# Kernel tuning notes

Measured on AMD Instinct MI355X. Metric: run time of the kernel, lower is better.

Reference implementation:

```python
import jax, jax.numpy as jnp
import numpy as np

EPS = 1e-6  # torch.nn.PairwiseDistance default eps: dist = ||x - y + eps||_2


def setup_inputs() -> dict:
    key = jax.random.key(0)
    k1, k2 = jax.random.split(key)
    samples = jax.random.normal(k1, (4096, 128), dtype=jnp.float32)   # batch of observations
    V = jax.random.uniform(k2, (65536, 128), dtype=jnp.float32)       # grown node codebook (torch.rand init)
    return {"samples": samples, "V": V}


def reference(samples, V):
    # activate_bmu, vectorized over the batch.
    # torch PairwiseDistance(p=2): d_n = || x - V_n + eps ||_2
    D = samples.shape[-1]
    x_sq = jnp.sum(samples * samples, axis=-1)        # [B]
    v_sq = jnp.sum(V * V, axis=-1)                    # [N]
    xv = jnp.einsum('bd,nd->bn', samples, V)          # [B, N]
    x_sum = jnp.sum(samples, axis=-1)                 # [B]
    v_sum = jnp.sum(V, axis=-1)                       # [N]
    sq = (x_sq[:, None] + v_sq[None, :] - 2.0 * xv
          + 2.0 * EPS * (x_sum[:, None] - v_sum[None, :]) + D * EPS * EPS)
    dists = jnp.sqrt(jnp.maximum(sq, 0.0))            # [B, N]
    # top-2 smallest distances -> BMU b, second BMU s
    neg_top2, idx = jax.lax.top_k(-dists, 2)          # [B, 2]
    b = idx[:, 0]
    s = idx[:, 1]
    a = jnp.exp(neg_top2[:, 0])                       # exp(-b_dist)
    return (b, s, a)
```

## Files before the change

### kernel.cpp

```cpp
#include <hip/hip_runtime.h>
#include <math.h>

#define NS 4096
#define NV 65536
#define DDIM 128
#define EPSV 1e-6f
#define NCHUNK 16
#define TILES_PER_CHUNK 32
#define NTILE 512
#define FLTMAX 3.402823466e+38f
#define IMAX 0x7fffffff

#define XSQ_F    0
#define XSUM_F   4096
#define PART_F   8192
#define D12_F    270336
#define T12_I    278528
#define CELL1_I  286720
#define CELL2_I  290816
#define WS_TILED_BYTE 1605632
#define TILE_BYTES 65536
#define TILE_STRIDE 66560

typedef __attribute__((ext_vector_type(8)))  __bf16        bf16x8;
typedef __attribute__((ext_vector_type(8)))  unsigned short ush8;
typedef __attribute__((ext_vector_type(4)))  unsigned short ush4;
typedef __attribute__((ext_vector_type(16))) float          f32x16;

typedef const __attribute__((address_space(1))) unsigned int* gp_t;
typedef __attribute__((address_space(3))) unsigned int*       lp_t;

__device__ __forceinline__ void async_cp16(const void* g, void* l) {
    __builtin_amdgcn_global_load_lds((gp_t)g, (lp_t)l, 16, 0, 0);
}

__device__ __forceinline__ unsigned short f2bf(float x) {
    unsigned u = __builtin_bit_cast(unsigned, x);
    u += 0x7FFFu + ((u >> 16) & 1u);
    return (unsigned short)(u >> 16);
}
__device__ __forceinline__ float bf2f(unsigned short h) {
    unsigned u = ((unsigned)h) << 16;
    return __builtin_bit_cast(float, u);
}

__device__ __forceinline__ void merge2t(float& d1, int& i1, float& d2, int& i2,
                                        float d, int i) {
    bool b1 = (d < d1) || (d == d1 && i < i1);
    bool b2 = (d < d2) || (d == d2 && i < i2);
    if (b1) { d2 = d1; i2 = i1; d1 = d; i1 = i; }
    else if (b2) { d2 = d; i2 = i; }
}

__device__ __forceinline__ void load_bfrag(const float* __restrict__ samples,
                                           int srow, int q, ush8* bh, ush8* bl) {
    const float4* s4 = (const float4*)samples;
    #pragma unroll
    for (int s = 0; s < 8; s++) {
        float4 x0 = s4[(size_t)srow * 32 + s * 4 + q * 2];
        float4 x1 = s4[(size_t)srow * 32 + s * 4 + q * 2 + 1];
        float xs[8] = {x0.x, x0.y, x0.z, x0.w, x1.x, x1.y, x1.z, x1.w};
        #pragma unroll
        for (int j = 0; j < 8; j++) {
            float y = -2.0f * xs[j];
            unsigned short hh = f2bf(y);
            bh[s][j] = hh;
            bl[s][j] = f2bf(y - bf2f(hh));
        }
    }
}

__device__ __forceinline__ void tile_mfma(const char* __restrict__ lds,
                                          const ush8* bh, const ush8* bl,
                                          int q, int l31, f32x16 acc[4]) {
    #pragma unroll
    for (int mi = 0; mi < 4; mi++) {
        const char* cjb = lds + TILE_BYTES + (size_t)(mi * 32 + 4 * q) * 4;
        float4 c0 = *(const float4*)(cjb);
        float4 c1 = *(const float4*)(cjb + 32);
        float4 c2 = *(const float4*)(cjb + 64);
        float4 c3 = *(const float4*)(cjb + 96);
        acc[mi][0] = c0.x;  acc[mi][1] = c0.y;  acc[mi][2] = c0.z;  acc[mi][3] = c0.w;
        acc[mi][4] = c1.x;  acc[mi][5] = c1.y;  acc[mi][6] = c1.z;  acc[mi][7] = c1.w;
        acc[mi][8] = c2.x;  acc[mi][9] = c2.y;  acc[mi][10] = c2.z; acc[mi][11] = c2.w;
        acc[mi][12] = c3.x; acc[mi][13] = c3.y; acc[mi][14] = c3.z; acc[mi][15] = c3.w;
    }
    #pragma unroll
    for (int s = 0; s < 8; s++) {
        bf16x8 bhs = __builtin_bit_cast(bf16x8, bh[s]);
        bf16x8 bls = __builtin_bit_cast(bf16x8, bl[s]);
        #pragma unroll
        for (int mi = 0; mi < 4; mi++) {
            bf16x8 ah = *(const bf16x8*)(lds + (size_t)((((s * 2 + 0) * 2 + q) * 128) + mi * 32 + l31) * 16);
            bf16x8 al = *(const bf16x8*)(lds + (size_t)((((s * 2 + 1) * 2 + q) * 128) + mi * 32 + l31) * 16);
            acc[mi] = __builtin_amdgcn_mfma_f32_32x32x16_bf16(ah, bhs, acc[mi], 0, 0, 0);
            acc[mi] = __builtin_amdgcn_mfma_f32_32x32x16_bf16(ah, bls, acc[mi], 0, 0, 0);
            acc[mi] = __builtin_amdgcn_mfma_f32_32x32x16_bf16(al, bhs, acc[mi], 0, 0, 0);
        }
    }
}

__global__ void vq_prep(const float* __restrict__ samples,
                        const float* __restrict__ V,
                        char* __restrict__ ws) {
    __shared__ float tf[128 * 132];
    float* ws_f = (float*)ws;
    const int b = blockIdx.x;
    const int tid = threadIdx.x;
    if (b >= NV / 128) {
        int row = (b - NV / 128) * 4 + (tid >> 6);
        int lane = tid & 63;
        float2 v = ((const float2*)(samples + (size_t)row * DDIM))[lane];
        float s = v.x + v.y;
        float q = v.x * v.x + v.y * v.y;
        #pragma unroll
        for (int off = 32; off >= 1; off >>= 1) {
            s += __shfl_xor(s, off);
            q += __shfl_xor(q, off);
        }
        if (lane == 0) { ws_f[XSQ_F + row] = q; ws_f[XSUM_F + row] = s; }
        return;
    }
    const int tile = b;
    char* dst = ws + WS_TILED_BYTE + (size_t)tile * TILE_STRIDE;
    const float4* v4 = (const float4*)V;
    #pragma unroll
    for (int i = 0; i < 16; i++) {
        int flat = i * 256 + tid;
        int row = flat >> 5;
        int c4 = flat & 31;
        float4 g = v4[(size_t)(tile * 128 + row) * 32 + c4];
        *(float4*)&tf[row * 132 + c4 * 4] = g;
        float s = g.x + g.y + g.z + g.w;
        float q2 = g.x * g.x + g.y * g.y + g.z * g.z + g.w * g.w;
        #pragma unroll
        for (int off = 16; off >= 1; off >>= 1) {
            s += __shfl_xor(s, off);
            q2 += __shfl_xor(q2, off);
        }
        if ((tid & 31) == 0)
            *(float*)(dst + TILE_BYTES + row * 4) = q2 - 2.0f * EPSV * s;
    }
    __syncthreads();
    #pragma unroll
    for (int i = 0; i < 8; i++) {
        int task = i * 256 + tid;
        int row = task & 127;
        int sq = task >> 7;
        int s = sq >> 1, q = sq & 1;
        float4 lo = *(const float4*)&tf[row * 132 + s * 16 + q * 8];
        float4 hi = *(const float4*)&tf[row * 132 + s * 16 + q * 8 + 4];
        float xs[8] = {lo.x, lo.y, lo.z, lo.w, hi.x, hi.y, hi.z, hi.w};
        ush8 h, l;
        #pragma unroll
        for (int j = 0; j < 8; j++) {
            unsigned short hh = f2bf(xs[j]);
            h[j] = hh;
            l[j] = f2bf(xs[j] - bf2f(hh));
        }
        *(ush8*)(dst + (size_t)((((s * 2 + 0) * 2 + q) * 128) + row) * 16) = h;
        *(ush8*)(dst + (size_t)((((s * 2 + 1) * 2 + q) * 128) + row) * 16) = l;
    }
}

__device__ __forceinline__ void stage_tile512(const char* src, char* l, int tid) {
    #pragma unroll
    for (int i = 0; i < 8; i++) {
        int off = (i * 512 + tid) * 16;
        async_cp16(src + off, l + off);
    }
    if (tid < 64) {
        int off = TILE_BYTES + tid * 16;
        async_cp16(src + off, l + off);
    }
}

__global__ __launch_bounds__(512, 2)
void vq_gemm_topk(const float* __restrict__ samples, char* __restrict__ ws) {
    __shared__ __align__(16) char lds[2][TILE_STRIDE];
    const int tid = threadIdx.x;
    const int w = tid >> 6, lane = tid & 63;
    const int l31 = lane & 31, qb = lane >> 5;
    const int bid = blockIdx.x;
    const int g = bid >> 3;
    const int chunk = (bid & 7) * 2 + (g >> 4);
    const int st = g & 15;
    const int nrow = st * 256 + w * 32 + l31;

    const char* vbase = ws + WS_TILED_BYTE;
    const int tbase = chunk * TILES_PER_CHUNK;

    stage_tile512(vbase + (size_t)tbase * TILE_STRIDE, lds[0], tid);
    ush8 bh[8], bl[8];
    load_bfrag(samples, nrow, qb, bh, bl);
    __syncthreads();

    float D1 = FLTMAX, D2 = FLTMAX;
    int T1 = IMAX, T2 = IMAX;

    #pragma unroll 1
    for (int it = 0; it < TILES_PER_CHUNK; it++) {
        const int cur = it & 1;
        if (it + 1 < TILES_PER_CHUNK)
            stage_tile512(vbase + (size_t)(tbase + it + 1) * TILE_STRIDE,
                          lds[cur ^ 1], tid);
        f32x16 acc[4];
        tile_mfma(lds[cur], bh, bl, qb, l31, acc);
        float t1[4], t2[4];
        #pragma unroll
        for (int mi = 0; mi < 4; mi++) {
            t1[mi] = FLTMAX; t2[mi] = FLTMAX;
            #pragma unroll
            for (int r = 0; r < 16; r++) {
                float v = acc[mi][r];
                t2[mi] = fminf(t2[mi], fmaxf(t1[mi], v));
                t1[mi] = fminf(t1[mi], v);
            }
        }
        float tt1 = t1[0], tt2 = t2[0];
        #pragma unroll
        for (int mi = 1; mi < 4; mi++) {
            float tmp = fmaxf(tt1, t1[mi]);
            tt1 = fminf(tt1, t1[mi]);
            tt2 = fminf(fminf(tmp, tt2), t2[mi]);
        }
        const int tile = tbase + it;
        bool c1 = tt1 < D1;
        float m1 = fminf(D1, tt2);
        float m2 = fminf(D2, tt1);
        int T2a = (tt2 < D1) ? tile : T1;
        int T2b = (tt1 < D2) ? tile : T2;
        D2 = c1 ? m1 : m2;
        T2 = c1 ? T2a : T2b;
        T1 = c1 ? tile : T1;
        D1 = c1 ? tt1 : D1;
        __syncthreads();
    }

    {
        float od1 = __shfl_xor(D1, 32), od2 = __shfl_xor(D2, 32);
        int   ot1 = __shfl_xor(T1, 32), ot2 = __shfl_xor(T2, 32);
        merge2t(D1, T1, D2, T2, od1, ot1);
        merge2t(D1, T1, D2, T2, od2, ot2);
    }
    if (qb == 0) {
        float4* part = (float4*)((float*)ws + PART_F);
        part[(size_t)nrow * NCHUNK + chunk] =
            make_float4(D1, D2, (float)T1, (float)T2);
    }
}

__global__ void vq_merge(float* __restrict__ ws_f, float* __restrict__ out) {
    const int m = blockIdx.x * 256 + threadIdx.x;
    int* ws_i = (int*)ws_f;
    const float4* part = (const float4*)(ws_f + PART_F);
    float d1 = FLTMAX, d2 = FLTMAX;
    int t1 = IMAX, t2 = IMAX;
    #pragma unroll
    for (int c = 0; c < NCHUNK; c++) {
        float4 p = part[(size_t)m * NCHUNK + c];
        merge2t(d1, t1, d2, t2, p.x, (int)p.z);
        merge2t(d1, t1, d2, t2, p.y, (int)p.w);
    }
    ((float2*)(ws_f + D12_F))[m] = make_float2(d1, d2);
    ((int2*)(ws_i + T12_I))[m] = make_int2(t1, t2);
    ws_i[CELL1_I + m] = IMAX;
    ws_i[CELL2_I + m] = IMAX;
    float ci = ws_f[XSQ_F + m] + 2.0f * EPSV * ws_f[XSUM_F + m] + (float)DDIM * EPSV * EPSV;
    out[2 * NS + m] = expf(-sqrtf(fmaxf(ci + d1, 0.0f)));
}

__global__ __launch_bounds__(256)
void vq_recover(const float* __restrict__ samples, char* __restrict__ ws) {
    __shared__ __align__(16) char sbuf[TILE_STRIDE];
    __shared__ int list[NS];
    __shared__ int lcnt;
    const int tid = threadIdx.x;
    const int w = tid >> 6, lane = tid & 63;
    const int l31 = lane & 31, qb = lane >> 5;
    const int tile = blockIdx.x;
    int* ws_i = (int*)ws;
    float* ws_f = (float*)ws;

    const char* tsrc = ws + WS_TILED_BYTE + (size_t)tile * TILE_STRIDE;
    #pragma unroll
    for (int i = 0; i < 16; i++) {
        int off = (i * 256 + tid) * 16;
        async_cp16(tsrc + off, sbuf + off);
    }
    if (tid < 64) {
        int off = TILE_BYTES + tid * 16;
        async_cp16(tsrc + off, sbuf + off);
    }
    if (tid == 0) lcnt = 0;
    __syncthreads();
    const int2* t12 = (const int2*)(ws_i + T12_I);
    for (int i = tid; i < NS; i += 256) {
        int2 t = t12[i];
        if (t.x == tile || t.y == tile) {
            int p = atomicAdd(&lcnt, 1);
            list[p] = i;
        }
    }
    __syncthreads();
    const int cnt = lcnt;
    if (cnt == 0) return;

    const float2* d12 = (const float2*)(ws_f + D12_F);
    const float nanf_ = __int_as_float(0x7fc00000);

    for (int b0 = 0; b0 < cnt; b0 += 128) {
        int li = b0 + w * 32 + l31;
        bool valid = li < cnt;
        int m = valid ? list[li] : 0;
        ush8 bh[8], bl[8];
        load_bfrag(samples, m, qb, bh, bl);
        float d1t = nanf_, d2t = nanf_;
        if (valid) {
            float2 dt = d12[m];
            d1t = dt.x; d2t = dt.y;
        }
        f32x16 acc[4];
        tile_mfma(sbuf, bh, bl, qb, l31, acc);
        #pragma unroll
        for (int mi = 0; mi < 4; mi++) {
            #pragma unroll
            for (int r = 0; r < 16; r++) {
                float v = acc[mi][r];
                int idx = tile * 128 + mi * 32 + (r & 3) + 8 * (r >> 2) + 4 * qb;
                if (v == d1t) {
                    int old = atomicMin(&ws_i[CELL1_I + m], idx);
                    int loser = old > idx ? old : idx;
                    atomicMin(&ws_i[CELL2_I + m], loser);
                } else if (v == d2t) {
                    atomicMin(&ws_i[CELL2_I + m], idx);
                }
            }
        }
    }
}

__global__ void vq_finalize(const char* __restrict__ ws, float* __restrict__ out) {
    const int m = blockIdx.x * 256 + threadIdx.x;
    const int* ws_i = (const int*)ws;
    out[m]      = (float)ws_i[CELL1_I + m];
    out[NS + m] = (float)ws_i[CELL2_I + m];
}

extern "C" void kernel_launch(void* const* d_in, const int* in_sizes, int n_in,
                              void* d_out, int out_size, void* d_ws, size_t ws_size,
                              hipStream_t stream) {
    (void)in_sizes; (void)n_in; (void)out_size; (void)ws_size;
    const float* samples = (const float*)d_in[0];
    const float* V = (const float*)d_in[1];
    float* out = (float*)d_out;
    float* ws_f = (float*)d_ws;
    char*  ws_b = (char*)d_ws;

    vq_prep<<<dim3(NV / 128 + NS / 4), 256, 0, stream>>>(samples, V, ws_b);
    vq_gemm_topk<<<dim3((NS / 256) * NCHUNK), 512, 0, stream>>>(samples, ws_b);
    vq_merge<<<dim3(NS / 256), 256, 0, stream>>>(ws_f, out);
    vq_recover<<<dim3(NTILE), 256, 0, stream>>>(samples, ws_b);
    vq_finalize<<<dim3(NS / 256), 256, 0, stream>>>(ws_b, out);
}
```

Before: 291.5 us.

## Retile GEMM warps to 64 samples by half-tile codebook rows for fragment reuse

Each warp now covers two 32-sample groups and half of the codebook tile's four 32-row M-blocks, instead of one sample group and all four M-blocks. Each A fragment read from LDS now feeds MFMAs for two sample groups, which halves LDS reads of the codebook tile per MFMA. Per-warp top-2 results for the two column halves are merged through LDS scratch after the loop. The cost is twice the B-fragment registers per lane, which may add register pressure and hurt occupancy at launch bounds (512,2), plus an extra synchronisation and merge step at the end.

```diff
diff --git a/kernel.cpp b/kernel.cpp
--- a/kernel.cpp
+++ b/kernel.cpp
@@ -185,18 +185,21 @@
     const int g = bid >> 3;
     const int chunk = (bid & 7) * 2 + (g >> 4);
     const int st = g & 15;
-    const int nrow = st * 256 + w * 32 + l31;
+    const int sg4 = w >> 1;
+    const int chalf = w & 1;
+    const int nrow0 = st * 256 + sg4 * 64 + l31;
 
     const char* vbase = ws + WS_TILED_BYTE;
     const int tbase = chunk * TILES_PER_CHUNK;
 
     stage_tile512(vbase + (size_t)tbase * TILE_STRIDE, lds[0], tid);
-    ush8 bh[8], bl[8];
-    load_bfrag(samples, nrow, qb, bh, bl);
-    __syncthreads();
-
-    float D1 = FLTMAX, D2 = FLTMAX;
-    int T1 = IMAX, T2 = IMAX;
+    ush8 bh0[8], bl0[8], bh1[8], bl1[8];
+    load_bfrag(samples, nrow0, qb, bh0, bl0);
+    load_bfrag(samples, nrow0 + 32, qb, bh1, bl1);
+    __syncthreads();
+
+    float D1[2] = {FLTMAX, FLTMAX}, D2[2] = {FLTMAX, FLTMAX};
+    int T1[2] = {IMAX, IMAX}, T2[2] = {IMAX, IMAX};
 
     #pragma unroll 1
     for (int it = 0; it < TILES_PER_CHUNK; it++) {
@@ -204,49 +207,96 @@
         if (it + 1 < TILES_PER_CHUNK)
             stage_tile512(vbase + (size_t)(tbase + it + 1) * TILE_STRIDE,
                           lds[cur ^ 1], tid);
-        f32x16 acc[4];
-        tile_mfma(lds[cur], bh, bl, qb, l31, acc);
-        float t1[4], t2[4];
-        #pragma unroll
-        for (int mi = 0; mi < 4; mi++) {
-            t1[mi] = FLTMAX; t2[mi] = FLTMAX;
+        const char* L = lds[cur];
+        f32x16 acc[2][2];
+        #pragma unroll
+        for (int mj = 0; mj < 2; mj++) {
+            const int mi = chalf * 2 + mj;
+            const char* cjb = L + TILE_BYTES + (size_t)(mi * 32 + 4 * qb) * 4;
+            float4 c0 = *(const float4*)(cjb);
+            float4 c1 = *(const float4*)(cjb + 32);
+            float4 c2 = *(const float4*)(cjb + 64);
+            float4 c3 = *(const float4*)(cjb + 96);
+            #pragma unroll
+            for (int gg = 0; gg < 2; gg++) {
+                acc[gg][mj][0] = c0.x;  acc[gg][mj][1] = c0.y;  acc[gg][mj][2] = c0.z;  acc[gg][mj][3] = c0.w;
+                acc[gg][mj][4] = c1.x;  acc[gg][mj][5] = c1.y;  acc[gg][mj][6] = c1.z;  acc[gg][mj][7] = c1.w;
+                acc[gg][mj][8] = c2.x;  acc[gg][mj][9] = c2.y;  acc[gg][mj][10] = c2.z; acc[gg][mj][11] = c2.w;
+                acc[gg][mj][12] = c3.x; acc[gg][mj][13] = c3.y; acc[gg][mj][14] = c3.z; acc[gg][mj][15] = c3.w;
+            }
+        }
+        #pragma unroll
+        for (int s = 0; s < 8; s++) {
+            bf16x8 b0h = __builtin_bit_cast(bf16x8, bh0[s]);
+            bf16x8 b0l = __builtin_bit_cast(bf16x8, bl0[s]);
+            bf16x8 b1h = __builtin_bit_cast(bf16x8, bh1[s]);
+            bf16x8 b1l = __builtin_bit_cast(bf16x8, bl1[s]);
+            #pragma unroll
+            for (int mj = 0; mj < 2; mj++) {
+                const int mi = chalf * 2 + mj;
+                bf16x8 ah = *(const bf16x8*)(L + (size_t)((((s * 2 + 0) * 2 + qb) * 128) + mi * 32 + l31) * 16);
+                bf16x8 al = *(const bf16x8*)(L + (size_t)((((s * 2 + 1) * 2 + qb) * 128) + mi * 32 + l31) * 16);
+                acc[0][mj] = __builtin_amdgcn_mfma_f32_32x32x16_bf16(ah, b0h, acc[0][mj], 0, 0, 0);
+                acc[0][mj] = __builtin_amdgcn_mfma_f32_32x32x16_bf16(ah, b0l, acc[0][mj], 0, 0, 0);
+                acc[0][mj] = __builtin_amdgcn_mfma_f32_32x32x16_bf16(al, b0h, acc[0][mj], 0, 0, 0);
+                acc[1][mj] = __builtin_amdgcn_mfma_f32_32x32x16_bf16(ah, b1h, acc[1][mj], 0, 0, 0);
+                acc[1][mj] = __builtin_amdgcn_mfma_f32_32x32x16_bf16(ah, b1l, acc[1][mj], 0, 0, 0);
+                acc[1][mj] = __builtin_amdgcn_mfma_f32_32x32x16_bf16(al, b1h, acc[1][mj], 0, 0, 0);
+            }
+        }
+        const int tile = tbase + it;
+        #pragma unroll
+        for (int gg = 0; gg < 2; gg++) {
+            float t1 = FLTMAX, t2 = FLTMAX, u1 = FLTMAX, u2 = FLTMAX;
             #pragma unroll
             for (int r = 0; r < 16; r++) {
-                float v = acc[mi][r];
-                t2[mi] = fminf(t2[mi], fmaxf(t1[mi], v));
-                t1[mi] = fminf(t1[mi], v);
+                float v = acc[gg][0][r];
+                t2 = fminf(t2, fmaxf(t1, v));
+                t1 = fminf(t1, v);
+                float v2 = acc[gg][1][r];
+                u2 = fminf(u2, fmaxf(u1, v2));
+                u1 = fminf(u1, v2);
             }
-        }
-        float tt1 = t1[0], tt2 = t2[0];
-        #pragma unroll
-        for (int mi = 1; mi < 4; mi++) {
-            float tmp = fmaxf(tt1, t1[mi]);
-            tt1 = fminf(tt1, t1[mi]);
-            tt2 = fminf(fminf(tmp, tt2), t2[mi]);
-        }
-        const int tile = tbase + it;
-        bool c1 = tt1 < D1;
-        float m1 = fminf(D1, tt2);
-        float m2 = fminf(D2, tt1);
-        int T2a = (tt2 < D1) ? tile : T1;
-        int T2b = (tt1 < D2) ? tile : T2;
-        D2 = c1 ? m1 : m2;
-        T2 = c1 ? T2a : T2b;
-        T1 = c1 ? tile : T1;
-        D1 = c1 ? tt1 : D1;
+            float tmp = fmaxf(t1, u1);
+            t1 = fminf(t1, u1);
+            t2 = fminf(fminf(tmp, t2), u2);
+            bool c1 = t1 < D1[gg];
+            float m1 = fminf(D1[gg], t2);
+            float m2 = fminf(D2[gg], t1);
+            int T2a = (t2 < D1[gg]) ? tile : T1[gg];
+            int T2b = (t1 < D2[gg]) ? tile : T2[gg];
+            D2[gg] = c1 ? m1 : m2;
+            T2[gg] = c1 ? T2a : T2b;
+            T1[gg] = c1 ? tile : T1[gg];
+            D1[gg] = c1 ? t1 : D1[gg];
+        }
         __syncthreads();
     }
 
-    {
-        float od1 = __shfl_xor(D1, 32), od2 = __shfl_xor(D2, 32);
-        int   ot1 = __shfl_xor(T1, 32), ot2 = __shfl_xor(T2, 32);
-        merge2t(D1, T1, D2, T2, od1, ot1);
-        merge2t(D1, T1, D2, T2, od2, ot2);
-    }
-    if (qb == 0) {
+    #pragma unroll
+    for (int gg = 0; gg < 2; gg++) {
+        float od1 = __shfl_xor(D1[gg], 32), od2 = __shfl_xor(D2[gg], 32);
+        int   ot1 = __shfl_xor(T1[gg], 32), ot2 = __shfl_xor(T2[gg], 32);
+        merge2t(D1[gg], T1[gg], D2[gg], T2[gg], od1, ot1);
+        merge2t(D1[gg], T1[gg], D2[gg], T2[gg], od2, ot2);
+    }
+    __syncthreads();
+    float4* scratch = (float4*)lds[0];
+    if (chalf == 1 && qb == 0) {
+        scratch[sg4 * 64 + l31]      = make_float4(D1[0], D2[0], (float)T1[0], (float)T2[0]);
+        scratch[sg4 * 64 + 32 + l31] = make_float4(D1[1], D2[1], (float)T1[1], (float)T2[1]);
+    }
+    __syncthreads();
+    if (chalf == 0 && qb == 0) {
         float4* part = (float4*)((float*)ws + PART_F);
-        part[(size_t)nrow * NCHUNK + chunk] =
-            make_float4(D1, D2, (float)T1, (float)T2);
+        #pragma unroll
+        for (int gg = 0; gg < 2; gg++) {
+            float4 o = scratch[sg4 * 64 + gg * 32 + l31];
+            merge2t(D1[gg], T1[gg], D2[gg], T2[gg], o.x, (int)o.z);
+            merge2t(D1[gg], T1[gg], D2[gg], T2[gg], o.y, (int)o.w);
+            part[(size_t)(st * 256 + sg4 * 64 + gg * 32 + l31) * NCHUNK + chunk] =
+                make_float4(D1[gg], D2[gg], (float)T1[gg], (float)T2[gg]);
+        }
     }
 }
 
```

Measured after the change: 316.2 us. 8.5% more time.

## Split each tile's M dimension across wave halves, single-buffer LDS, double grid

Applied to the files above, without the earlier changes.

The GEMM+top-2 kernel now gives each block 128 sample rows instead of 256. Its 8 waves split into two groups, each covering half of the tile's 128 codebook rows (2 MFMA row-blocks instead of 4). The two groups' top-2 results are merged through LDS before the partial is written. LDS is single-buffered with a sync-stage-sync sequence instead of double-buffered prefetch, and launch bounds rise to 4 blocks per CU. The goal is more blocks and occupancy and lower register pressure, but the tile load is no longer overlapped with compute within a block, and each tile is now loaded twice as often overall.

```diff
diff --git a/kernel.cpp b/kernel.cpp
--- a/kernel.cpp
+++ b/kernel.cpp
@@ -175,22 +175,24 @@
     }
 }
 
-__global__ __launch_bounds__(512, 2)
+__global__ __launch_bounds__(512, 4)
 void vq_gemm_topk(const float* __restrict__ samples, char* __restrict__ ws) {
-    __shared__ __align__(16) char lds[2][TILE_STRIDE];
+    __shared__ __align__(16) char lds[TILE_STRIDE];
     const int tid = threadIdx.x;
     const int w = tid >> 6, lane = tid & 63;
     const int l31 = lane & 31, qb = lane >> 5;
+    const int ws3 = w & 3;
+    const int wq  = w >> 2;
     const int bid = blockIdx.x;
     const int g = bid >> 3;
-    const int chunk = (bid & 7) * 2 + (g >> 4);
-    const int st = g & 15;
-    const int nrow = st * 256 + w * 32 + l31;
+    const int chunk = (bid & 7) * 2 + (g >> 5);
+    const int st = g & 31;
+    const int nrow = st * 128 + ws3 * 32 + l31;
 
     const char* vbase = ws + WS_TILED_BYTE;
     const int tbase = chunk * TILES_PER_CHUNK;
 
-    stage_tile512(vbase + (size_t)tbase * TILE_STRIDE, lds[0], tid);
+    stage_tile512(vbase + (size_t)tbase * TILE_STRIDE, lds, tid);
     ush8 bh[8], bl[8];
     load_bfrag(samples, nrow, qb, bh, bl);
     __syncthreads();
@@ -200,41 +202,64 @@
 
     #pragma unroll 1
     for (int it = 0; it < TILES_PER_CHUNK; it++) {
-        const int cur = it & 1;
-        if (it + 1 < TILES_PER_CHUNK)
-            stage_tile512(vbase + (size_t)(tbase + it + 1) * TILE_STRIDE,
-                          lds[cur ^ 1], tid);
-        f32x16 acc[4];
-        tile_mfma(lds[cur], bh, bl, qb, l31, acc);
-        float t1[4], t2[4];
-        #pragma unroll
-        for (int mi = 0; mi < 4; mi++) {
-            t1[mi] = FLTMAX; t2[mi] = FLTMAX;
+        f32x16 acc[2];
+        #pragma unroll
+        for (int mj = 0; mj < 2; mj++) {
+            const int mi = wq * 2 + mj;
+            const char* cjb = lds + TILE_BYTES + (size_t)(mi * 32 + 4 * qb) * 4;
+            float4 c0 = *(const float4*)(cjb);
+            float4 c1 = *(const float4*)(cjb + 32);
+            float4 c2 = *(const float4*)(cjb + 64);
+            float4 c3 = *(const float4*)(cjb + 96);
+            acc[mj][0] = c0.x;  acc[mj][1] = c0.y;  acc[mj][2] = c0.z;  acc[mj][3] = c0.w;
+            acc[mj][4] = c1.x;  acc[mj][5] = c1.y;  acc[mj][6] = c1.z;  acc[mj][7] = c1.w;
+            acc[mj][8] = c2.x;  acc[mj][9] = c2.y;  acc[mj][10] = c2.z; acc[mj][11] = c2.w;
+            acc[mj][12] = c3.x; acc[mj][13] = c3.y; acc[mj][14] = c3.z; acc[mj][15] = c3.w;
+        }
+        #pragma unroll
+        for (int s = 0; s < 8; s++) {
+            bf16x8 bhs = __builtin_bit_cast(bf16x8, bh[s]);
+            bf16x8 bls = __builtin_bit_cast(bf16x8, bl[s]);
             #pragma unroll
-            for (int r = 0; r < 16; r++) {
-                float v = acc[mi][r];
-                t2[mi] = fminf(t2[mi], fmaxf(t1[mi], v));
-                t1[mi] = fminf(t1[mi], v);
+            for (int mj = 0; mj < 2; mj++) {
+                const int mi = wq * 2 + mj;
+                bf16x8 ah = *(const bf16x8*)(lds + (size_t)((((s * 2 + 0) * 2 + qb) * 128) + mi * 32 + l31) * 16);
+                bf16x8 al = *(const bf16x8*)(lds + (size_t)((((s * 2 + 1) * 2 + qb) * 128) + mi * 32 + l31) * 16);
+                acc[mj] = __builtin_amdgcn_mfma_f32_32x32x16_bf16(ah, bhs, acc[mj], 0, 0, 0);
+                acc[mj] = __builtin_amdgcn_mfma_f32_32x32x16_bf16(ah, bls, acc[mj], 0, 0, 0);
+                acc[mj] = __builtin_amdgcn_mfma_f32_32x32x16_bf16(al, bhs, acc[mj], 0, 0, 0);
             }
         }
-        float tt1 = t1[0], tt2 = t2[0];
-        #pragma unroll
-        for (int mi = 1; mi < 4; mi++) {
-            float tmp = fmaxf(tt1, t1[mi]);
-            tt1 = fminf(tt1, t1[mi]);
-            tt2 = fminf(fminf(tmp, tt2), t2[mi]);
-        }
         const int tile = tbase + it;
-        bool c1 = tt1 < D1;
-        float m1 = fminf(D1, tt2);
-        float m2 = fminf(D2, tt1);
-        int T2a = (tt2 < D1) ? tile : T1;
-        int T2b = (tt1 < D2) ? tile : T2;
+        float t1 = FLTMAX, t2 = FLTMAX, u1 = FLTMAX, u2 = FLTMAX;
+        #pragma unroll
+        for (int r = 0; r < 16; r++) {
+            float v0 = acc[0][r];
+            t2 = fminf(t2, fmaxf(t1, v0));
+            t1 = fminf(t1, v0);
+            float v1 = acc[1][r];
+            u2 = fminf(u2, fmaxf(u1, v1));
+            u1 = fminf(u1, v1);
+        }
+        {
+            float tmp = fmaxf(t1, u1);
+            t1 = fminf(t1, u1);
+            t2 = fminf(fminf(tmp, t2), u2);
+        }
+        bool c1 = t1 < D1;
+        float m1 = fminf(D1, t2);
+        float m2 = fminf(D2, t1);
+        int T2a = (t2 < D1) ? tile : T1;
+        int T2b = (t1 < D2) ? tile : T2;
         D2 = c1 ? m1 : m2;
         T2 = c1 ? T2a : T2b;
         T1 = c1 ? tile : T1;
-        D1 = c1 ? tt1 : D1;
+        D1 = c1 ? t1 : D1;
         __syncthreads();
+        if (it + 1 < TILES_PER_CHUNK) {
+            stage_tile512(vbase + (size_t)(tbase + it + 1) * TILE_STRIDE, lds, tid);
+            __syncthreads();
+        }
     }
 
     {
@@ -243,7 +268,14 @@
         merge2t(D1, T1, D2, T2, od1, ot1);
         merge2t(D1, T1, D2, T2, od2, ot2);
     }
-    if (qb == 0) {
+    float4* scratch = (float4*)lds;
+    if (wq == 1 && qb == 0)
+        scratch[ws3 * 32 + l31] = make_float4(D1, D2, (float)T1, (float)T2);
+    __syncthreads();
+    if (wq == 0 && qb == 0) {
+        float4 o = scratch[ws3 * 32 + l31];
+        merge2t(D1, T1, D2, T2, o.x, (int)o.z);
+        merge2t(D1, T1, D2, T2, o.y, (int)o.w);
         float4* part = (float4*)((float*)ws + PART_F);
         part[(size_t)nrow * NCHUNK + chunk] =
             make_float4(D1, D2, (float)T1, (float)T2);
@@ -358,7 +390,7 @@
     char*  ws_b = (char*)d_ws;
 
     vq_prep<<<dim3(NV / 128 + NS / 4), 256, 0, stream>>>(samples, V, ws_b);
-    vq_gemm_topk<<<dim3((NS / 256) * NCHUNK), 512, 0, stream>>>(samples, ws_b);
+    vq_gemm_topk<<<dim3((NS / 128) * NCHUNK), 512, 0, stream>>>(samples, ws_b);
     vq_merge<<<dim3(NS / 256), 256, 0, stream>>>(ws_f, out);
     vq_recover<<<dim3(NTILE), 256, 0, stream>>>(samples, ws_b);
     vq_finalize<<<dim3(NS / 256), 256, 0, stream>>>(ws_b, out);
```

Measured after the change: 386.5 us. +32.6%, slower.

## Software-pipeline tile MFMA with previous tile's top-2 reduction; use fmed3 for second-min

Applied to the files above, without the earlier changes.

Restructures the tile loop so the MFMA for tile i+1 is issued before the top-2 reduction over tile i's accumulators, using two accumulator sets (A/B) and a manually unrolled two-tile loop. The point is to let the VALU min/max work overlap with matrix-core execution instead of waiting on MFMA results. The second-minimum update also switches to a single fmed3 instruction instead of a min of a max. Keeping two accumulator sets doubles live accumulator registers, which may raise register pressure and lower occupancy.

```diff
diff --git a/kernel.cpp b/kernel.cpp
--- a/kernel.cpp
+++ b/kernel.cpp
@@ -70,12 +70,12 @@
     }
 }
 
-__device__ __forceinline__ void tile_mfma(const char* __restrict__ lds,
+__device__ __forceinline__ void tile_mfma(const char* __restrict__ base,
                                           const ush8* bh, const ush8* bl,
                                           int q, int l31, f32x16 acc[4]) {
     #pragma unroll
     for (int mi = 0; mi < 4; mi++) {
-        const char* cjb = lds + TILE_BYTES + (size_t)(mi * 32 + 4 * q) * 4;
+        const char* cjb = base + TILE_BYTES + (size_t)(mi * 32 + 4 * q) * 4;
         float4 c0 = *(const float4*)(cjb);
         float4 c1 = *(const float4*)(cjb + 32);
         float4 c2 = *(const float4*)(cjb + 64);
@@ -91,13 +91,44 @@
         bf16x8 bls = __builtin_bit_cast(bf16x8, bl[s]);
         #pragma unroll
         for (int mi = 0; mi < 4; mi++) {
-            bf16x8 ah = *(const bf16x8*)(lds + (size_t)((((s * 2 + 0) * 2 + q) * 128) + mi * 32 + l31) * 16);
-            bf16x8 al = *(const bf16x8*)(lds + (size_t)((((s * 2 + 1) * 2 + q) * 128) + mi * 32 + l31) * 16);
+            bf16x8 ah = *(const bf16x8*)(base + (size_t)((((s * 2 + 0) * 2 + q) * 128) + mi * 32 + l31) * 16);
+            bf16x8 al = *(const bf16x8*)(base + (size_t)((((s * 2 + 1) * 2 + q) * 128) + mi * 32 + l31) * 16);
             acc[mi] = __builtin_amdgcn_mfma_f32_32x32x16_bf16(ah, bhs, acc[mi], 0, 0, 0);
             acc[mi] = __builtin_amdgcn_mfma_f32_32x32x16_bf16(ah, bls, acc[mi], 0, 0, 0);
             acc[mi] = __builtin_amdgcn_mfma_f32_32x32x16_bf16(al, bhs, acc[mi], 0, 0, 0);
         }
     }
+}
+
+__device__ __forceinline__ void top2_acc(const f32x16 acc[4], int tile,
+                                         float& D1, float& D2, int& T1, int& T2) {
+    float t1[4], t2[4];
+    #pragma unroll
+    for (int mi = 0; mi < 4; mi++) {
+        t1[mi] = FLTMAX; t2[mi] = FLTMAX;
+        #pragma unroll
+        for (int r = 0; r < 16; r++) {
+            float v = acc[mi][r];
+            t2[mi] = __builtin_amdgcn_fmed3f(t1[mi], t2[mi], v);
+            t1[mi] = fminf(t1[mi], v);
+        }
+    }
+    float tt1 = t1[0], tt2 = t2[0];
+    #pragma unroll
+    for (int mi = 1; mi < 4; mi++) {
+        float tmp = fmaxf(tt1, t1[mi]);
+        tt1 = fminf(tt1, t1[mi]);
+        tt2 = fminf(fminf(tmp, tt2), t2[mi]);
+    }
+    bool c1 = tt1 < D1;
+    float m1 = fminf(D1, tt2);
+    float m2 = fminf(D2, tt1);
+    int T2a = (tt2 < D1) ? tile : T1;
+    int T2b = (tt1 < D2) ? tile : T2;
+    D2 = c1 ? m1 : m2;
+    T2 = c1 ? T2a : T2b;
+    T1 = c1 ? tile : T1;
+    D1 = c1 ? tt1 : D1;
 }
 
 __global__ void vq_prep(const float* __restrict__ samples,
@@ -194,48 +225,29 @@
     ush8 bh[8], bl[8];
     load_bfrag(samples, nrow, qb, bh, bl);
     __syncthreads();
+    stage_tile512(vbase + (size_t)(tbase + 1) * TILE_STRIDE, lds[1], tid);
+    f32x16 accA[4], accB[4];
+    tile_mfma(lds[0], bh, bl, qb, l31, accA);
+    __syncthreads();
 
     float D1 = FLTMAX, D2 = FLTMAX;
     int T1 = IMAX, T2 = IMAX;
 
     #pragma unroll 1
-    for (int it = 0; it < TILES_PER_CHUNK; it++) {
-        const int cur = it & 1;
-        if (it + 1 < TILES_PER_CHUNK)
-            stage_tile512(vbase + (size_t)(tbase + it + 1) * TILE_STRIDE,
-                          lds[cur ^ 1], tid);
-        f32x16 acc[4];
-        tile_mfma(lds[cur], bh, bl, qb, l31, acc);
-        float t1[4], t2[4];
-        #pragma unroll
-        for (int mi = 0; mi < 4; mi++) {
-            t1[mi] = FLTMAX; t2[mi] = FLTMAX;
-            #pragma unroll
-            for (int r = 0; r < 16; r++) {
-                float v = acc[mi][r];
-                t2[mi] = fminf(t2[mi], fmaxf(t1[mi], v));
-                t1[mi] = fminf(t1[mi], v);
-            }
-        }
-        float tt1 = t1[0], tt2 = t2[0];
-        #pragma unroll
-        for (int mi = 1; mi < 4; mi++) {
-            float tmp = fmaxf(tt1, t1[mi]);
-            tt1 = fminf(tt1, t1[mi]);
-            tt2 = fminf(fminf(tmp, tt2), t2[mi]);
-        }
-        const int tile = tbase + it;
-        bool c1 = tt1 < D1;
-        float m1 = fminf(D1, tt2);
-        float m2 = fminf(D2, tt1);
-        int T2a = (tt2 < D1) ? tile : T1;
-        int T2b = (tt1 < D2) ? tile : T2;
-        D2 = c1 ? m1 : m2;
-        T2 = c1 ? T2a : T2b;
-        T1 = c1 ? tile : T1;
-        D1 = c1 ? tt1 : D1;
+    for (int p = 0; p < 15; p++) {
+        const int te = tbase + 2 * p;
+        stage_tile512(vbase + (size_t)(te + 2) * TILE_STRIDE, lds[0], tid);
+        tile_mfma(lds[1], bh, bl, qb, l31, accB);
+        top2_acc(accA, te, D1, D2, T1, T2);
         __syncthreads();
-    }
+        stage_tile512(vbase + (size_t)(te + 3) * TILE_STRIDE, lds[1], tid);
+        tile_mfma(lds[0], bh, bl, qb, l31, accA);
+        top2_acc(accB, te + 1, D1, D2, T1, T2);
+        __syncthreads();
+    }
+    tile_mfma(lds[1], bh, bl, qb, l31, accB);
+    top2_acc(accA, tbase + 30, D1, D2, T1, T2);
+    top2_acc(accB, tbase + 31, D1, D2, T1, T2);
 
     {
         float od1 = __shfl_xor(D1, 32), od2 = __shfl_xor(D2, 32);
```

Result: slower. 302.9 us (+3.9%).
